# Performance work log

Measured on AMD Instinct MI355X. Metric: run time of the kernel, lower is better.

Reference implementation:

```python
import jax, jax.numpy as jnp
import numpy as np

B, S, E, H = 256, 512, 256, 256
START = 0
MASK_VAL = -100000.0


def _u(k, shape, s):
    return jax.random.uniform(k, shape, jnp.float32, -s, s)


def setup_inputs() -> dict:
    key = jax.random.key(0)
    ks = jax.random.split(key, 14)
    se = 1.0 / np.sqrt(E)
    sh = 1.0 / np.sqrt(H)
    return {
        'inputs': jax.random.uniform(ks[0], (B, S, 2), jnp.float32),
        'W_embed': _u(ks[1], (2, E), se),
        'enc_Wih': _u(ks[2], (4 * H, E), sh),
        'enc_Whh': _u(ks[3], (4 * H, H), sh),
        'enc_bih': _u(ks[4], (4 * H,), sh),
        'enc_bhh': _u(ks[5], (4 * H,), sh),
        'dec_Wih': _u(ks[6], (4 * H, E), sh),
        'dec_Whh': _u(ks[7], (4 * H, H), sh),
        'dec_bih': _u(ks[8], (4 * H,), sh),
        'dec_bhh': _u(ks[9], (4 * H,), sh),
        'Wq': _u(ks[10], (H, H), sh),
        'Wref': _u(ks[11], (H, H), sh),
        'v': _u(ks[12], (H,), sh),
    }


def lstm_cell(x, h, c, Wih, Whh, bih, bhh):
    # PyTorch gate order: input, forget, cell(g), output
    gates = x @ Wih.T + h @ Whh.T + bih + bhh
    i, f, g, o = jnp.split(gates, 4, axis=-1)
    c = jax.nn.sigmoid(f) * c + jax.nn.sigmoid(i) * jnp.tanh(g)
    h = jax.nn.sigmoid(o) * jnp.tanh(c)
    return h, c


def reference(inputs, W_embed, enc_Wih, enc_Whh, enc_bih, enc_bhh,
              dec_Wih, dec_Whh, dec_bih, dec_bhh, Wq, Wref, v):
    # GraphEmbedding: per-node linear projection of 2-D coords -> [B,S,E]
    emb = jnp.einsum('bsi,ie->bse', inputs, W_embed)

    # Encoder LSTM over the sequence
    def enc_step(carry, x):
        h, c = carry
        h, c = lstm_cell(x, h, c, enc_Wih, enc_Whh, enc_bih, enc_bhh)
        return (h, c), h

    h0 = jnp.zeros((B, H), emb.dtype)
    c0 = jnp.zeros((B, H), emb.dtype)
    (h, c), enc_out = jax.lax.scan(enc_step, (h0, c0), jnp.swapaxes(emb, 0, 1))
    enc_out = jnp.swapaxes(enc_out, 0, 1)  # [B,S,H]

    # Pointer attention: precompute W_ref projection of encoder outputs
    ref_proj = enc_out @ Wref.T  # [B,S,H]

    mask0 = jnp.zeros((B, S), bool).at[:, START].set(True)
    dec_in0 = emb[:, START, :]
    batch_ix = jnp.arange(B)

    def dec_step(carry, key):
        h, c, x, mask = carry
        h, c = lstm_cell(x, h, c, dec_Wih, dec_Whh, dec_bih, dec_bhh)
        q = (h @ Wq.T)[:, None, :]                            # [B,1,H]
        logits = jnp.einsum('bsh,h->bs', jnp.tanh(q + ref_proj), v)
        logits = jnp.where(mask, MASK_VAL, logits)
        chosen = jax.random.categorical(key, logits)          # [B]
        logp = jax.nn.log_softmax(logits, axis=-1)
        lp = jnp.take_along_axis(logp, chosen[:, None], axis=1)[:, 0]
        mask = mask.at[batch_ix, chosen].set(True)
        x = emb[batch_ix, chosen]
        return (h, c, x, mask), (lp, chosen)

    keys = jax.random.split(jax.random.key(1), S - 1)
    _, (lps, idxs) = jax.lax.scan(dec_step, (h, c, dec_in0, mask0), keys)

    logprobs = jnp.swapaxes(lps, 0, 1)                        # [B,S-1]
    start_col = jnp.full((B, 1), START, dtype=idxs.dtype)
    indices = jnp.concatenate([start_col, jnp.swapaxes(idxs, 0, 1)], axis=1)  # [B,S]
    return logprobs, indices
```

## Files before the change

kernel.cpp:

```cpp
#include <hip/hip_runtime.h>
#include <stdint.h>
#include <math.h>

#define Bn 256
#define Sn 512
#define En 256
#define Hn 256
#define Gn 1024
#define NSTEP 511
#define MASK_VAL -100000.0

#define PARTITIONABLE 1

__device__ __forceinline__ uint32_t rotl32(uint32_t v, int d) {
  return (v << d) | (v >> (32 - d));
}

__device__ __forceinline__ void threefry2x32(uint32_t k0, uint32_t k1,
                                             uint32_t x0, uint32_t x1,
                                             uint32_t& o0, uint32_t& o1) {
  const uint32_t ks2 = k0 ^ k1 ^ 0x1BD11BDAu;
  x0 += k0; x1 += k1;
  x0 += x1; x1 = rotl32(x1, 13); x1 ^= x0;
  x0 += x1; x1 = rotl32(x1, 15); x1 ^= x0;
  x0 += x1; x1 = rotl32(x1, 26); x1 ^= x0;
  x0 += x1; x1 = rotl32(x1,  6); x1 ^= x0;
  x0 += k1; x1 += ks2 + 1u;
  x0 += x1; x1 = rotl32(x1, 17); x1 ^= x0;
  x0 += x1; x1 = rotl32(x1, 29); x1 ^= x0;
  x0 += x1; x1 = rotl32(x1, 16); x1 ^= x0;
  x0 += x1; x1 = rotl32(x1, 24); x1 ^= x0;
  x0 += ks2; x1 += k0 + 2u;
  x0 += x1; x1 = rotl32(x1, 13); x1 ^= x0;
  x0 += x1; x1 = rotl32(x1, 15); x1 ^= x0;
  x0 += x1; x1 = rotl32(x1, 26); x1 ^= x0;
  x0 += x1; x1 = rotl32(x1,  6); x1 ^= x0;
  x0 += k0; x1 += k1 + 3u;
  x0 += x1; x1 = rotl32(x1, 17); x1 ^= x0;
  x0 += x1; x1 = rotl32(x1, 29); x1 ^= x0;
  x0 += x1; x1 = rotl32(x1, 16); x1 ^= x0;
  x0 += x1; x1 = rotl32(x1, 24); x1 ^= x0;
  x0 += k1; x1 += ks2 + 4u;
  x0 += x1; x1 = rotl32(x1, 13); x1 ^= x0;
  x0 += x1; x1 = rotl32(x1, 15); x1 ^= x0;
  x0 += x1; x1 = rotl32(x1, 26); x1 ^= x0;
  x0 += x1; x1 = rotl32(x1,  6); x1 ^= x0;
  x0 += ks2; x1 += k0 + 5u;
  o0 = x0; o1 = x1;
}

__device__ __forceinline__ uint32_t random_word(uint32_t k0, uint32_t k1, uint32_t n) {
#if PARTITIONABLE
  uint32_t o0, o1;
  threefry2x32(k0, k1, 0u, n, o0, o1);
  return o0 ^ o1;
#else
  const uint32_t half = (Bn * Sn) / 2;
  uint32_t lane = (n < half) ? n : (n - half);
  uint32_t o0, o1;
  threefry2x32(k0, k1, lane, lane + half, o0, o1);
  return (n < half) ? o0 : o1;
#endif
}

__device__ __forceinline__ double sigmoid64(double x) {
  return 1.0 / (1.0 + exp(-x));
}

__global__ __launch_bounds__(256) void k_wihe(const float* __restrict__ wemb,
                                              const float* __restrict__ wih,
                                              const float* __restrict__ bih,
                                              const float* __restrict__ bhh,
                                              double* __restrict__ wihe,
                                              double* __restrict__ bias) {
  int j = blockIdx.x * blockDim.x + threadIdx.x;
  if (j >= Gn) return;
  double a0 = 0.0, a1 = 0.0;
  for (int e = 0; e < En; ++e) {
    double w = (double)wih[j * En + e];
    a0 += (double)wemb[e] * w;
    a1 += (double)wemb[En + e] * w;
  }
  wihe[j] = a0;
  wihe[Gn + j] = a1;
  bias[j] = (double)bih[j] + (double)bhh[j];
}

__global__ __launch_bounds__(256) void k_keys(uint32_t* __restrict__ keys) {
  int j = blockIdx.x * blockDim.x + threadIdx.x;
  if (j >= NSTEP) return;
#if PARTITIONABLE
  uint32_t o0, o1;
  threefry2x32(0u, 1u, 0u, (uint32_t)j, o0, o1);
  keys[2 * j] = o0; keys[2 * j + 1] = o1;
#else
  uint32_t w[2];
  #pragma unroll
  for (int q = 0; q < 2; ++q) {
    uint32_t m = (uint32_t)(2 * j + q);
    uint32_t lane = (m < NSTEP) ? m : (m - NSTEP);
    uint32_t o0, o1;
    threefry2x32(0u, 1u, lane, lane + NSTEP, o0, o1);
    w[q] = (m < NSTEP) ? o0 : o1;
  }
  keys[2 * j] = w[0]; keys[2 * j + 1] = w[1];
#endif
}

__global__ __launch_bounds__(256) void k_t32(const float* __restrict__ src,
                                             float* __restrict__ dst) {
  int idx = blockIdx.x * blockDim.x + threadIdx.x;
  int k = idx >> 8, j = idx & 255;
  dst[idx] = src[j * Hn + k];
}

__global__ __launch_bounds__(256) void k_t32w(const float* __restrict__ src,
                                              float* __restrict__ dst) {
  int idx = blockIdx.x * blockDim.x + threadIdx.x;
  int k = idx >> 10, j = idx & 1023;
  dst[idx] = src[j * Hn + k];
}

__global__ __launch_bounds__(256) void k_init(float* __restrict__ out) {
  int idx = blockIdx.x * blockDim.x + threadIdx.x;
  if (idx < Bn) out[Bn * NSTEP + idx * Sn] = 0.0f;
}

struct AttnS {
  double qpart[4][256];
  double p2[2][512];
  double sl[512];
  double zz[512];
  double sg[512];
  float  qf[256];
  float  vbuf[256];
};

__global__ __launch_bounds__(1024, 4) void k_main(
    const float* __restrict__ inp,
    const double* __restrict__ wihe_e, const double* __restrict__ bias_e,
    const float* __restrict__ whhT_e,
    const double* __restrict__ wihe_d, const double* __restrict__ bias_d,
    const float* __restrict__ whhT_d,
    const float* __restrict__ wrefT, const float* __restrict__ wqT,
    const float* __restrict__ v,
    float* __restrict__ refT,
    const uint32_t* __restrict__ keys,
    float* __restrict__ out) {
  __shared__ double sh_h[Hn];
  __shared__ double sh_g[Gn];
  __shared__ AttnS at;
  __shared__ int smask[Sn];

  const int b   = blockIdx.x;
  const int tid = threadIdx.x;
  const int w   = tid >> 6;
  const int l   = tid & 63;

  const double bj_e = bias_e[tid], w0e = wihe_e[tid], w1e = wihe_e[Gn + tid];
  const double bj_d = bias_d[tid], w0d = wihe_d[tid], w1d = wihe_d[Gn + tid];

  double creg = 0.0;
  if (tid < Hn) sh_h[tid] = 0.0;
  if (tid < Sn) smask[tid] = (tid == 0) ? 1 : 0;
  if (tid < Hn) at.vbuf[tid] = v[tid];
  __syncthreads();

  const float* wcol_e = whhT_e + tid;
  const float* wcol_d = whhT_d + tid;
  const int part = tid >> 8, tcol = tid & 255;

  for (int s = 0; s < Sn; ++s) {
    {
      double x0 = (double)inp[((size_t)b * Sn + s) * 2 + 0];
      double x1 = (double)inp[((size_t)b * Sn + s) * 2 + 1];
      double acc = bj_e + x0 * w0e + x1 * w1e;
      #pragma unroll 8
      for (int k = 0; k < Hn; ++k)
        acc += sh_h[k] * (double)wcol_e[(size_t)k << 10];
      sh_g[tid] = acc;
    }
    __syncthreads();
    if (tid < Hn) {
      double gi = sh_g[tid];
      double gf = sh_g[256 + tid];
      double gg = sh_g[512 + tid];
      double go = sh_g[768 + tid];
      double cn = sigmoid64(gf) * creg + sigmoid64(gi) * tanh(gg);
      double hn = sigmoid64(go) * tanh(cn);
      creg = cn;
      sh_h[tid] = hn;
    }
    __syncthreads();
    {
      double racc = 0.0;
      #pragma unroll 8
      for (int i = 0; i < 64; ++i) {
        int k = part * 64 + i;
        racc += sh_h[k] * (double)wrefT[(size_t)k * Hn + tcol];
      }
      at.qpart[part][tcol] = racc;
    }
    __syncthreads();
    if (tid < Hn) {
      double r = (at.qpart[0][tid] + at.qpart[1][tid]) +
                 (at.qpart[2][tid] + at.qpart[3][tid]);
      refT[((size_t)b * Hn + tid) * Sn + s] = (float)r;
    }
  }

  int ch = 0;
  for (int t = 0; t < NSTEP; ++t) {
    {
      const uint32_t k0 = keys[2 * t], k1 = keys[2 * t + 1];
      if (tid < Sn) {
        uint32_t wrd = random_word(k0, k1, (uint32_t)(b * Sn + tid));
        float uf = __uint_as_float((wrd >> 9) | 0x3f800000u) - 1.0f;
        uf = fmaxf(uf, 1.17549435e-38f);
        at.sg[tid] = -log(-log((double)uf));
      }
    }
    {
      double x0 = (double)inp[((size_t)b * Sn + ch) * 2 + 0];
      double x1 = (double)inp[((size_t)b * Sn + ch) * 2 + 1];
      double acc = bj_d + x0 * w0d + x1 * w1d;
      #pragma unroll 8
      for (int k = 0; k < Hn; ++k)
        acc += sh_h[k] * (double)wcol_d[(size_t)k << 10];
      sh_g[tid] = acc;
    }
    __syncthreads();
    if (tid < Hn) {
      double gi = sh_g[tid];
      double gf = sh_g[256 + tid];
      double gg = sh_g[512 + tid];
      double go = sh_g[768 + tid];
      double cn = sigmoid64(gf) * creg + sigmoid64(gi) * tanh(gg);
      double hn = sigmoid64(go) * tanh(cn);
      creg = cn;
      sh_h[tid] = hn;
    }
    __syncthreads();
    {
      double qa = 0.0;
      #pragma unroll 8
      for (int i = 0; i < 64; ++i) {
        int k = part * 64 + i;
        qa += sh_h[k] * (double)wqT[(size_t)k * Hn + tcol];
      }
      at.qpart[part][tcol] = qa;
    }
    __syncthreads();
    if (tid < Hn) {
      double q = (at.qpart[0][tid] + at.qpart[1][tid]) +
                 (at.qpart[2][tid] + at.qpart[3][tid]);
      at.qf[tid] = (float)q;
    }
    __syncthreads();
    {
      const int sE = tid & 511, ph = tid >> 9;
      const float* rT = refT + ((size_t)b * Hn + ph * 128) * Sn + sE;
      double la = 0.0;
      for (int c = 0; c < 16; ++c) {
        float st[8];
        #pragma unroll
        for (int i = 0; i < 8; ++i)
          st[i] = rT[(size_t)(c * 8 + i) * Sn];
        #pragma unroll
        for (int i = 0; i < 8; ++i) {
          int t2 = ph * 128 + c * 8 + i;
          float qv = at.qf[t2];
          double vv = (double)at.vbuf[t2];
          la += vv * (double)tanhf(qv + st[i]);
        }
      }
      at.p2[ph][sE] = la;
    }
    __syncthreads();
    if (tid < Sn) {
      double lg = smask[tid] ? (double)MASK_VAL
                             : (at.p2[0][tid] + at.p2[1][tid]);
      at.sl[tid] = lg;
      at.zz[tid] = lg + at.sg[tid];
    }
    __syncthreads();
    {
      double bz = at.zz[l]; int bi = l;
      #pragma unroll
      for (int k = 1; k < 8; ++k) {
        int s2 = l + k * 64;
        double z2 = at.zz[s2];
        if (z2 > bz || (z2 == bz && s2 < bi)) { bz = z2; bi = s2; }
      }
      #pragma unroll
      for (int m = 32; m >= 1; m >>= 1) {
        double oz = __shfl_xor(bz, m);
        int    oi = __shfl_xor(bi, m);
        if (oz > bz || (oz == bz && oi < bi)) { bz = oz; bi = oi; }
      }
      ch = bi;
    }
    if (w == 1) {
      double bm = at.sl[l];
      #pragma unroll
      for (int k = 1; k < 8; ++k) bm = fmax(bm, at.sl[l + k * 64]);
      #pragma unroll
      for (int m = 32; m >= 1; m >>= 1) bm = fmax(bm, __shfl_xor(bm, m));
      double ps = 0.0;
      #pragma unroll
      for (int k = 0; k < 8; ++k) ps += exp(at.sl[l + k * 64] - bm);
      #pragma unroll
      for (int m = 32; m >= 1; m >>= 1) ps += __shfl_xor(ps, m);
      if (l == 0) {
        double lse = bm + log(ps);
        double lp = at.sl[ch] - lse;
        out[(size_t)b * NSTEP + t] = (float)lp;
        out[(size_t)Bn * NSTEP + (size_t)b * Sn + (t + 1)] = (float)ch;
        smask[ch] = 1;
      }
    }
  }
}

extern "C" void kernel_launch(void* const* d_in, const int* in_sizes, int n_in,
                              void* d_out, int out_size, void* d_ws, size_t ws_size,
                              hipStream_t stream) {
  const float* inp  = (const float*)d_in[0];
  const float* wemb = (const float*)d_in[1];
  const float* eWih = (const float*)d_in[2];
  const float* eWhh = (const float*)d_in[3];
  const float* ebih = (const float*)d_in[4];
  const float* ebhh = (const float*)d_in[5];
  const float* dWih = (const float*)d_in[6];
  const float* dWhh = (const float*)d_in[7];
  const float* dbih = (const float*)d_in[8];
  const float* dbhh = (const float*)d_in[9];
  const float* Wq   = (const float*)d_in[10];
  const float* Wref = (const float*)d_in[11];
  const float* v    = (const float*)d_in[12];
  float* out = (float*)d_out;

  char* ws = (char*)d_ws;
  size_t off = 0;
  auto alloc = [&](size_t bytes) -> void* {
    void* p = (void*)(ws + off);
    off += (bytes + 255) & ~(size_t)255;
    return p;
  };
  float*    refT   = (float*)   alloc((size_t)Bn * Sn * Hn * sizeof(float));
  float*    whhT_e = (float*)   alloc((size_t)Hn * Gn * sizeof(float));
  float*    whhT_d = (float*)   alloc((size_t)Hn * Gn * sizeof(float));
  float*    wqT    = (float*)   alloc((size_t)Hn * Hn * sizeof(float));
  float*    wrefT  = (float*)   alloc((size_t)Hn * Hn * sizeof(float));
  double*   wihe_e = (double*)  alloc(2 * Gn * sizeof(double));
  double*   wihe_d = (double*)  alloc(2 * Gn * sizeof(double));
  double*   bias_e = (double*)  alloc(Gn * sizeof(double));
  double*   bias_d = (double*)  alloc(Gn * sizeof(double));
  uint32_t* keys   = (uint32_t*)alloc(2 * NSTEP * sizeof(uint32_t));
  (void)ws_size; (void)in_sizes; (void)n_in; (void)out_size;

  k_wihe<<<Gn / 256, 256, 0, stream>>>(wemb, eWih, ebih, ebhh, wihe_e, bias_e);
  k_wihe<<<Gn / 256, 256, 0, stream>>>(wemb, dWih, dbih, dbhh, wihe_d, bias_d);
  k_keys<<<2, 256, 0, stream>>>(keys);
  k_t32<<<(Hn * Hn) / 256, 256, 0, stream>>>(Wq, wqT);
  k_t32<<<(Hn * Hn) / 256, 256, 0, stream>>>(Wref, wrefT);
  k_t32w<<<(Hn * Gn) / 256, 256, 0, stream>>>(eWhh, whhT_e);
  k_t32w<<<(Hn * Gn) / 256, 256, 0, stream>>>(dWhh, whhT_d);
  k_init<<<1, 256, 0, stream>>>(out);

  k_main<<<Bn, 1024, 0, stream>>>(
      inp, wihe_e, bias_e, whhT_e, wihe_d, bias_d, whhT_d,
      wrefT, wqT, v, refT, keys, out);
}
```

Baseline: 28.16 ms.

## Use fast float attention logits with exact fallback when argmax gap is small

Computes attention logits in float with a fast exp-based tanh and only recomputes them in double with tanhf when the top-two Gumbel-perturbed scores are within a small threshold. It also vectorizes the hidden-state reads in the LSTM matvecs as double2 and makes the chosen index wave-uniform via readfirstlane. The goal is cheaper transcendental and accumulation work in the per-step attention. In exchange, the log-probabilities come from the lower-precision logits whenever the gap is large, and the threshold heuristic may not guarantee bitwise-equal choices.

```diff
diff --git a/kernel.cpp b/kernel.cpp
--- a/kernel.cpp
+++ b/kernel.cpp
@@ -11,6 +11,8 @@
 #define MASK_VAL -100000.0
 
 #define PARTITIONABLE 1
+
+#define GAP_TRIG 5e-4
 
 __device__ __forceinline__ uint32_t rotl32(uint32_t v, int d) {
   return (v << d) | (v >> (32 - d));
@@ -67,6 +69,11 @@
   return 1.0 / (1.0 + exp(-x));
 }
 
+__device__ __forceinline__ float tanh_fast(float x) {
+  float e = __expf(2.0f * x);
+  return 1.0f - 2.0f / (e + 1.0f);
+}
+
 __global__ __launch_bounds__(256) void k_wihe(const float* __restrict__ wemb,
                                               const float* __restrict__ wih,
                                               const float* __restrict__ bih,
@@ -147,7 +154,7 @@
     float* __restrict__ refT,
     const uint32_t* __restrict__ keys,
     float* __restrict__ out) {
-  __shared__ double sh_h[Hn];
+  __shared__ __align__(16) double sh_h[Hn];
   __shared__ double sh_g[Gn];
   __shared__ AttnS at;
   __shared__ int smask[Sn];
@@ -175,9 +182,12 @@
       double x0 = (double)inp[((size_t)b * Sn + s) * 2 + 0];
       double x1 = (double)inp[((size_t)b * Sn + s) * 2 + 1];
       double acc = bj_e + x0 * w0e + x1 * w1e;
-      #pragma unroll 8
-      for (int k = 0; k < Hn; ++k)
-        acc += sh_h[k] * (double)wcol_e[(size_t)k << 10];
+      #pragma unroll 4
+      for (int k = 0; k < Hn; k += 2) {
+        double2 hv = *(const double2*)&sh_h[k];
+        acc += hv.x * (double)wcol_e[(size_t)k << 10];
+        acc += hv.y * (double)wcol_e[(size_t)(k + 1) << 10];
+      }
       sh_g[tid] = acc;
     }
     __syncthreads();
@@ -221,12 +231,16 @@
       }
     }
     {
-      double x0 = (double)inp[((size_t)b * Sn + ch) * 2 + 0];
-      double x1 = (double)inp[((size_t)b * Sn + ch) * 2 + 1];
+      int col = __builtin_amdgcn_readfirstlane(ch);
+      double x0 = (double)inp[((size_t)b * Sn + col) * 2 + 0];
+      double x1 = (double)inp[((size_t)b * Sn + col) * 2 + 1];
       double acc = bj_d + x0 * w0d + x1 * w1d;
-      #pragma unroll 8
-      for (int k = 0; k < Hn; ++k)
-        acc += sh_h[k] * (double)wcol_d[(size_t)k << 10];
+      #pragma unroll 4
+      for (int k = 0; k < Hn; k += 2) {
+        double2 hv = *(const double2*)&sh_h[k];
+        acc += hv.x * (double)wcol_d[(size_t)k << 10];
+        acc += hv.y * (double)wcol_d[(size_t)(k + 1) << 10];
+      }
       sh_g[tid] = acc;
     }
     __syncthreads();
@@ -257,10 +271,10 @@
       at.qf[tid] = (float)q;
     }
     __syncthreads();
-    {
-      const int sE = tid & 511, ph = tid >> 9;
+    const int sE = tid & 511, ph = tid >> 9;
+    {
       const float* rT = refT + ((size_t)b * Hn + ph * 128) * Sn + sE;
-      double la = 0.0;
+      float la = 0.0f;
       for (int c = 0; c < 16; ++c) {
         float st[8];
         #pragma unroll
@@ -269,12 +283,10 @@
         #pragma unroll
         for (int i = 0; i < 8; ++i) {
           int t2 = ph * 128 + c * 8 + i;
-          float qv = at.qf[t2];
-          double vv = (double)at.vbuf[t2];
-          la += vv * (double)tanhf(qv + st[i]);
+          la += at.vbuf[t2] * tanh_fast(at.qf[t2] + st[i]);
         }
       }
-      at.p2[ph][sE] = la;
+      at.p2[ph][sE] = (double)la;
     }
     __syncthreads();
     if (tid < Sn) {
@@ -284,13 +296,63 @@
       at.zz[tid] = lg + at.sg[tid];
     }
     __syncthreads();
-    {
-      double bz = at.zz[l]; int bi = l;
+    double z1, z2; int i1;
+    {
+      z1 = at.zz[l]; i1 = l; z2 = -1.0e300;
       #pragma unroll
       for (int k = 1; k < 8; ++k) {
         int s2 = l + k * 64;
-        double z2 = at.zz[s2];
-        if (z2 > bz || (z2 == bz && s2 < bi)) { bz = z2; bi = s2; }
+        double zc = at.zz[s2];
+        if (zc > z1 || (zc == z1 && s2 < i1)) { z2 = z1; z1 = zc; i1 = s2; }
+        else if (zc > z2) z2 = zc;
+      }
+      #pragma unroll
+      for (int m = 32; m >= 1; m >>= 1) {
+        double oz1 = __shfl_xor(z1, m);
+        int    oi1 = __shfl_xor(i1, m);
+        double oz2 = __shfl_xor(z2, m);
+        if (oz1 > z1 || (oz1 == z1 && oi1 < i1)) {
+          z2 = fmax(z1, oz2); z1 = oz1; i1 = oi1;
+        } else {
+          z2 = fmax(z2, oz1);
+        }
+      }
+    }
+    if (z1 - z2 >= GAP_TRIG) {
+      ch = i1;
+    } else {
+      {
+        const float* rT = refT + ((size_t)b * Hn + ph * 128) * Sn + sE;
+        double la = 0.0;
+        for (int c = 0; c < 16; ++c) {
+          float st[8];
+          #pragma unroll
+          for (int i = 0; i < 8; ++i)
+            st[i] = rT[(size_t)(c * 8 + i) * Sn];
+          #pragma unroll
+          for (int i = 0; i < 8; ++i) {
+            int t2 = ph * 128 + c * 8 + i;
+            float qv = at.qf[t2];
+            double vv = (double)at.vbuf[t2];
+            la += vv * (double)tanhf(qv + st[i]);
+          }
+        }
+        at.p2[ph][sE] = la;
+      }
+      __syncthreads();
+      if (tid < Sn) {
+        double lg = smask[tid] ? (double)MASK_VAL
+                               : (at.p2[0][tid] + at.p2[1][tid]);
+        at.sl[tid] = lg;
+        at.zz[tid] = lg + at.sg[tid];
+      }
+      __syncthreads();
+      double bz = at.zz[l]; int bi = l;
+      #pragma unroll
+      for (int k = 1; k < 8; ++k) {
+        int s2 = l + k * 64;
+        double zc = at.zz[s2];
+        if (zc > bz || (zc == bz && s2 < bi)) { bz = zc; bi = s2; }
       }
       #pragma unroll
       for (int m = 32; m >= 1; m >>= 1) {
```

Result: slower. 29.51 ms (+4.8%).

## Fuse gate activations into matvec, keep mask in registers, drop a barrier

Applied to the files above, without the earlier changes.

Applies sigmoid/tanh per gate in the thread that computes it, so the cell-update threads only do the combine. The shared smask array is replaced by per-lane bitmask registers, and logits are computed in registers. This removes the sl/zz shared arrays and one __syncthreads per decoder step, and the Gumbel noise buffer is double-buffered by step parity. The h loads are vectorized as double2 and the chosen index goes through readfirstlane. All of this aims to shorten the serial per-step latency, at the cost of more register pressure and more transcendental work across all 1024 threads.

```diff
diff --git a/kernel.cpp b/kernel.cpp
--- a/kernel.cpp
+++ b/kernel.cpp
@@ -129,9 +129,7 @@
 struct AttnS {
   double qpart[4][256];
   double p2[2][512];
-  double sl[512];
-  double zz[512];
-  double sg[512];
+  double sg[2][512];
   float  qf[256];
   float  vbuf[256];
 };
@@ -147,22 +145,21 @@
     float* __restrict__ refT,
     const uint32_t* __restrict__ keys,
     float* __restrict__ out) {
-  __shared__ double sh_h[Hn];
+  __shared__ __align__(16) double sh_h[Hn];
   __shared__ double sh_g[Gn];
   __shared__ AttnS at;
-  __shared__ int smask[Sn];
 
   const int b   = blockIdx.x;
   const int tid = threadIdx.x;
   const int w   = tid >> 6;
   const int l   = tid & 63;
+  const int gsel = tid >> 8;
 
   const double bj_e = bias_e[tid], w0e = wihe_e[tid], w1e = wihe_e[Gn + tid];
   const double bj_d = bias_d[tid], w0d = wihe_d[tid], w1d = wihe_d[Gn + tid];
 
   double creg = 0.0;
   if (tid < Hn) sh_h[tid] = 0.0;
-  if (tid < Sn) smask[tid] = (tid == 0) ? 1 : 0;
   if (tid < Hn) at.vbuf[tid] = v[tid];
   __syncthreads();
 
@@ -175,19 +172,22 @@
       double x0 = (double)inp[((size_t)b * Sn + s) * 2 + 0];
       double x1 = (double)inp[((size_t)b * Sn + s) * 2 + 1];
       double acc = bj_e + x0 * w0e + x1 * w1e;
-      #pragma unroll 8
-      for (int k = 0; k < Hn; ++k)
-        acc += sh_h[k] * (double)wcol_e[(size_t)k << 10];
-      sh_g[tid] = acc;
+      #pragma unroll 4
+      for (int k = 0; k < Hn; k += 2) {
+        double2 hv = *(const double2*)&sh_h[k];
+        acc += hv.x * (double)wcol_e[(size_t)k << 10];
+        acc += hv.y * (double)wcol_e[(size_t)(k + 1) << 10];
+      }
+      sh_g[tid] = (gsel == 2) ? tanh(acc) : sigmoid64(acc);
     }
     __syncthreads();
     if (tid < Hn) {
-      double gi = sh_g[tid];
-      double gf = sh_g[256 + tid];
-      double gg = sh_g[512 + tid];
-      double go = sh_g[768 + tid];
-      double cn = sigmoid64(gf) * creg + sigmoid64(gi) * tanh(gg);
-      double hn = sigmoid64(go) * tanh(cn);
+      double ti = sh_g[tid];
+      double tf = sh_g[256 + tid];
+      double tg = sh_g[512 + tid];
+      double to = sh_g[768 + tid];
+      double cn = tf * creg + ti * tg;
+      double hn = to * tanh(cn);
       creg = cn;
       sh_h[tid] = hn;
     }
@@ -210,33 +210,39 @@
   }
 
   int ch = 0;
+  unsigned mbits = (l == 0) ? 1u : 0u;
   for (int t = 0; t < NSTEP; ++t) {
+    const int par = t & 1;
     {
       const uint32_t k0 = keys[2 * t], k1 = keys[2 * t + 1];
       if (tid < Sn) {
         uint32_t wrd = random_word(k0, k1, (uint32_t)(b * Sn + tid));
         float uf = __uint_as_float((wrd >> 9) | 0x3f800000u) - 1.0f;
         uf = fmaxf(uf, 1.17549435e-38f);
-        at.sg[tid] = -log(-log((double)uf));
-      }
-    }
-    {
-      double x0 = (double)inp[((size_t)b * Sn + ch) * 2 + 0];
-      double x1 = (double)inp[((size_t)b * Sn + ch) * 2 + 1];
+        at.sg[par][tid] = -log(-log((double)uf));
+      }
+    }
+    {
+      int col = __builtin_amdgcn_readfirstlane(ch);
+      double x0 = (double)inp[((size_t)b * Sn + col) * 2 + 0];
+      double x1 = (double)inp[((size_t)b * Sn + col) * 2 + 1];
       double acc = bj_d + x0 * w0d + x1 * w1d;
-      #pragma unroll 8
-      for (int k = 0; k < Hn; ++k)
-        acc += sh_h[k] * (double)wcol_d[(size_t)k << 10];
-      sh_g[tid] = acc;
+      #pragma unroll 4
+      for (int k = 0; k < Hn; k += 2) {
+        double2 hv = *(const double2*)&sh_h[k];
+        acc += hv.x * (double)wcol_d[(size_t)k << 10];
+        acc += hv.y * (double)wcol_d[(size_t)(k + 1) << 10];
+      }
+      sh_g[tid] = (gsel == 2) ? tanh(acc) : sigmoid64(acc);
     }
     __syncthreads();
     if (tid < Hn) {
-      double gi = sh_g[tid];
-      double gf = sh_g[256 + tid];
-      double gg = sh_g[512 + tid];
-      double go = sh_g[768 + tid];
-      double cn = sigmoid64(gf) * creg + sigmoid64(gi) * tanh(gg);
-      double hn = sigmoid64(go) * tanh(cn);
+      double ti = sh_g[tid];
+      double tf = sh_g[256 + tid];
+      double tg = sh_g[512 + tid];
+      double to = sh_g[768 + tid];
+      double cn = tf * creg + ti * tg;
+      double hn = to * tanh(cn);
       creg = cn;
       sh_h[tid] = hn;
     }
@@ -277,19 +283,20 @@
       at.p2[ph][sE] = la;
     }
     __syncthreads();
-    if (tid < Sn) {
-      double lg = smask[tid] ? (double)MASK_VAL
-                             : (at.p2[0][tid] + at.p2[1][tid]);
-      at.sl[tid] = lg;
-      at.zz[tid] = lg + at.sg[tid];
-    }
-    __syncthreads();
-    {
-      double bz = at.zz[l]; int bi = l;
+    double slv[8];
+    {
+      #pragma unroll
+      for (int k = 0; k < 8; ++k) {
+        int s2 = l + k * 64;
+        slv[k] = (mbits >> k) & 1u ? (double)MASK_VAL
+                                   : (at.p2[0][s2] + at.p2[1][s2]);
+      }
+      double bz = slv[0] + at.sg[par][l];
+      int bi = l;
       #pragma unroll
       for (int k = 1; k < 8; ++k) {
         int s2 = l + k * 64;
-        double z2 = at.zz[s2];
+        double z2 = slv[k] + at.sg[par][s2];
         if (z2 > bz || (z2 == bz && s2 < bi)) { bz = z2; bi = s2; }
       }
       #pragma unroll
@@ -301,24 +308,25 @@
       ch = bi;
     }
     if (w == 1) {
-      double bm = at.sl[l];
-      #pragma unroll
-      for (int k = 1; k < 8; ++k) bm = fmax(bm, at.sl[l + k * 64]);
+      double bm = slv[0];
+      #pragma unroll
+      for (int k = 1; k < 8; ++k) bm = fmax(bm, slv[k]);
       #pragma unroll
       for (int m = 32; m >= 1; m >>= 1) bm = fmax(bm, __shfl_xor(bm, m));
       double ps = 0.0;
       #pragma unroll
-      for (int k = 0; k < 8; ++k) ps += exp(at.sl[l + k * 64] - bm);
+      for (int k = 0; k < 8; ++k) ps += exp(slv[k] - bm);
       #pragma unroll
       for (int m = 32; m >= 1; m >>= 1) ps += __shfl_xor(ps, m);
       if (l == 0) {
         double lse = bm + log(ps);
-        double lp = at.sl[ch] - lse;
+        double slch = at.p2[0][ch] + at.p2[1][ch];
+        double lp = slch - lse;
         out[(size_t)b * NSTEP + t] = (float)lp;
         out[(size_t)Bn * NSTEP + (size_t)b * Sn + (t + 1)] = (float)ch;
-        smask[ch] = 1;
-      }
-    }
+      }
+    }
+    if ((ch & 63) == l) mbits |= 1u << (ch >> 6);
   }
 }
 
```

Measured after the change: 27.80 ms. Within noise of the previous version (-1.3%).
